# Performance work log

Measured on AMD Instinct MI355X. Metric: run time of the kernel, lower is better.

## Reference

```python
import jax, jax.numpy as jnp
import numpy as np

IN_FEATURES = 4096
OUT_FEATURES = 11008
GROUP_SIZE = 128
NUM_GROUPS = IN_FEATURES // GROUP_SIZE  # 32


def setup_inputs() -> dict:
    key = jax.random.key(0)
    k1, k2, k3, k4 = jax.random.split(key, 4)
    x = jax.random.normal(k1, (8192, IN_FEATURES), dtype=jnp.float32)
    # packed 4-bit weights: one uint8 byte holds two 4-bit values
    qweight = jax.random.randint(k2, (IN_FEATURES * OUT_FEATURES // 2,), 0, 256, dtype=jnp.int32)
    qzeros = jax.random.randint(k3, (OUT_FEATURES, NUM_GROUPS), 0, 16, dtype=jnp.int32)
    scales = jax.random.uniform(k4, (OUT_FEATURES, NUM_GROUPS), dtype=jnp.float32) * 0.01
    return {"x": x, "qweight": qweight, "qzeros": qzeros, "scales": scales}


def _dequantize(qweight, qzeros, scales):
    # unpack: low nibble first, then high nibble (matches stack([low, high], dim=1).view(-1))
    b = qweight.astype(jnp.int32)
    low = b & 15
    high = (b >> 4) & 15
    w = jnp.stack([low, high], axis=1).reshape(-1)  # [in*out]
    w = w[: OUT_FEATURES * IN_FEATURES].reshape(OUT_FEATURES, IN_FEATURES).astype(jnp.float32)
    # per-group dequant: (w - zero) * scale, groups along in_features
    w = w.reshape(OUT_FEATURES, NUM_GROUPS, GROUP_SIZE)
    w = (w - qzeros[:, :, None].astype(jnp.float32)) * scales[:, :, None]
    return w.reshape(OUT_FEATURES, IN_FEATURES)


def reference(x, qweight, qzeros, scales) -> jnp.ndarray:
    weight = _dequantize(qweight, qzeros, scales).astype(x.dtype)  # [out, in]
    # F.linear(x, W) = x @ W.T
    return jnp.einsum("bi,oi->bo", x, weight)
```

## Files before the change

### kernel.cpp

```cpp
#include <hip/hip_runtime.h>
#include <hip/hip_bf16.h>


#define IN_F   4096
#define OUT_F  11008
#define M_DIM  8192
#define NGROUP 32

typedef __bf16 bf16x8 __attribute__((ext_vector_type(8)));
typedef float  f32x4  __attribute__((ext_vector_type(4)));
typedef unsigned short u16;
typedef u16 u16x8v __attribute__((ext_vector_type(8)));

__device__ __forceinline__ u16 f2bf(float f) {
  union { float f; unsigned u; } v; v.f = f;
  unsigned u = v.u;
  return (u16)((u + 0x7fffu + ((u >> 16) & 1u)) >> 16);
}

__device__ __forceinline__ void gload_lds16(const void* gsrc, void* ldst) {
  __builtin_amdgcn_global_load_lds(
      (const __attribute__((address_space(1))) void*)gsrc,
      (__attribute__((address_space(3))) void*)ldst, 16, 0, 0);
}

__global__ __launch_bounds__(256) void dequant_w(const int* __restrict__ qw,
                                                 const int* __restrict__ qz,
                                                 const float* __restrict__ sc,
                                                 u16* __restrict__ W) {
  const int total = (IN_F / 2) * OUT_F / 4;
  int stride = gridDim.x * blockDim.x;
  for (int idx = blockIdx.x * blockDim.x + threadIdx.x; idx < total; idx += stride) {
    int j = idx << 2;
    int o = j >> 11;
    int g = (j >> 6) & 31;
    float z = (float)qz[(o << 5) + g];
    float s = sc[(o << 5) + g];
    int4 q = ((const int4*)qw)[idx];
    int qs0 = q.x, qs1 = q.y, qs2 = q.z, qs3 = q.w;
    u16x8v w;
    w[0] = f2bf(((float)(qs0 & 15) - z) * s);
    w[1] = f2bf(((float)((qs0 >> 4) & 15) - z) * s);
    w[2] = f2bf(((float)(qs1 & 15) - z) * s);
    w[3] = f2bf(((float)((qs1 >> 4) & 15) - z) * s);
    w[4] = f2bf(((float)(qs2 & 15) - z) * s);
    w[5] = f2bf(((float)((qs2 >> 4) & 15) - z) * s);
    w[6] = f2bf(((float)(qs3 & 15) - z) * s);
    w[7] = f2bf(((float)((qs3 >> 4) & 15) - z) * s);
    ((u16x8v*)W)[idx] = w;
  }
}

__global__ __launch_bounds__(256) void cvt_x(const float* __restrict__ x,
                                             u16* __restrict__ Xb) {
  const int total = M_DIM * IN_F / 8;
  int stride = gridDim.x * blockDim.x;
  for (int idx = blockIdx.x * blockDim.x + threadIdx.x; idx < total; idx += stride) {
    float4 a = ((const float4*)x)[idx * 2];
    float4 b = ((const float4*)x)[idx * 2 + 1];
    u16x8v v;
    v[0] = f2bf(a.x); v[1] = f2bf(a.y); v[2] = f2bf(a.z); v[3] = f2bf(a.w);
    v[4] = f2bf(b.x); v[5] = f2bf(b.y); v[6] = f2bf(b.z); v[7] = f2bf(b.w);
    ((u16x8v*)Xb)[idx] = v;
  }
}


#define BAR       __builtin_amdgcn_s_barrier()
#define LGKM0     asm volatile("s_waitcnt lgkmcnt(0)" ::: "memory")
#define VMCNT4    asm volatile("s_waitcnt vmcnt(4)" ::: "memory")
#define PRIO(p)   __builtin_amdgcn_s_setprio(p)

__global__ __launch_bounds__(512, 2) void gemm256(const u16* __restrict__ A,
                                                  const u16* __restrict__ B,
                                                  float* __restrict__ C) {
  constexpr int K = IN_F, N = OUT_F;
  constexpr int NT = K / 64;
  __shared__ __align__(16) u16 sA[2][256 * 64];
  __shared__ __align__(16) u16 sB[2][256 * 64];

  const int NTN = OUT_F / 256;
  const int NWG = (M_DIM / 256) * NTN;
  int bid = blockIdx.x;
  int wg  = (bid & 7) * (NWG / 8) + (bid >> 3);
  int tm = wg / NTN, tn = wg - tm * NTN;
  int m0 = tm * 256, n0 = tn * 256;

  int tid  = threadIdx.x;
  int lane = tid & 63;
  int wave = tid >> 6;
  int wr = wave >> 2, wc = wave & 3;

  int rstage = tid >> 3;
  int gslot  = ((tid & 7) ^ (rstage & 7)) << 3;
  int ldsoff = rstage * 64 + ((tid & 7) << 3);
  const u16* Ag = A + (size_t)(m0 + rstage) * K + gslot;
  const u16* Bg = B + (size_t)(n0 + rstage) * K + gslot;

#define STAGE_A(cb, h, kt) do {                                   \
    const u16* _g = Ag + (size_t)(h) * 128 * K + (kt) * 64;       \
    u16* _l = sA[cb] + (h) * 128 * 64 + ldsoff;                   \
    gload_lds16(_g, _l);                                          \
    gload_lds16(_g + (size_t)64 * K, _l + 64 * 64);               \
  } while (0)

#define STAGE_B(cb, h, kt) do {                                   \
    const u16* _g = Bg + (size_t)(h) * 128 * K + (kt) * 64;       \
    u16* _l = sB[cb] + (h) * 128 * 64 + ldsoff;                   \
    gload_lds16(_g, _l);                                          \
    gload_lds16(_g + (size_t)64 * K, _l + 64 * 64);               \
  } while (0)

  int q8  = lane >> 4;
  int sl0 = ((q8 ^ (lane & 7)) << 3);
  int sl1 = (((q8 | 4) ^ (lane & 7)) << 3);
  int abase = (wr * 128 + (lane & 15)) * 64;
  int bbase = (wc * 64 + (lane & 15)) * 64;

  bf16x8 a_[8], b0_[4], b1_[4];
  f32x4 acc[8][4] = {};

#define LDA(cb, mh) do {                                          \
    const u16* _p = sA[cb] + abase + (mh) * 4096;                 \
    a_[0] = *(const bf16x8*)(_p + sl0);                           \
    a_[1] = *(const bf16x8*)(_p + sl1);                           \
    a_[2] = *(const bf16x8*)(_p + 1024 + sl0);                    \
    a_[3] = *(const bf16x8*)(_p + 1024 + sl1);                    \
    a_[4] = *(const bf16x8*)(_p + 2048 + sl0);                    \
    a_[5] = *(const bf16x8*)(_p + 2048 + sl1);                    \
    a_[6] = *(const bf16x8*)(_p + 3072 + sl0);                    \
    a_[7] = *(const bf16x8*)(_p + 3072 + sl1);                    \
  } while (0)

#define LDB(cb, nh, dst) do {                                     \
    const u16* _p = sB[cb] + bbase + (nh) * 2048;                 \
    dst[0] = *(const bf16x8*)(_p + sl0);                          \
    dst[1] = *(const bf16x8*)(_p + sl1);                          \
    dst[2] = *(const bf16x8*)(_p + 1024 + sl0);                   \
    dst[3] = *(const bf16x8*)(_p + 1024 + sl1);                   \
  } while (0)

#define QUAD(mh, nh, bq) do {                                                  \
    _Pragma("unroll") for (int mf = 0; mf < 4; mf++)                           \
      _Pragma("unroll") for (int nf = 0; nf < 2; nf++) {                       \
        acc[(mh)*4+mf][(nh)*2+nf] = __builtin_amdgcn_mfma_f32_16x16x32_bf16(   \
            a_[mf*2+0], bq[nf*2+0], acc[(mh)*4+mf][(nh)*2+nf], 0, 0, 0);       \
        acc[(mh)*4+mf][(nh)*2+nf] = __builtin_amdgcn_mfma_f32_16x16x32_bf16(   \
            a_[mf*2+1], bq[nf*2+1], acc[(mh)*4+mf][(nh)*2+nf], 0, 0, 0);       \
      }                                                                        \
  } while (0)

#define TILE(c, u) do {                                           \
    int _ka = ((u) + 1) & (NT - 1), _kb = ((u) + 2) & (NT - 1);   \
                                                          \
    LDA(c, 0); LDB(c, 0, b0_); STAGE_A((c) ^ 1, 0, _ka);          \
    BAR; LGKM0; PRIO(1); QUAD(0, 0, b0_); PRIO(0); BAR;           \
                                                          \
    LDB(c, 1, b1_); STAGE_A((c) ^ 1, 1, _ka);                     \
    BAR; LGKM0; PRIO(1); QUAD(0, 1, b1_); PRIO(0); BAR;           \
                                                          \
    LDA(c, 1); STAGE_B(c, 0, _kb);                                \
    BAR; LGKM0; PRIO(1); QUAD(1, 1, b1_); PRIO(0); BAR;           \
                                                          \
    STAGE_B(c, 1, _kb);                                           \
    BAR; PRIO(1); QUAD(1, 0, b0_); PRIO(0); VMCNT4; BAR;          \
  } while (0)

  STAGE_A(0, 0, 0); STAGE_A(0, 1, 0);
  STAGE_B(0, 0, 0); STAGE_B(0, 1, 0);
  STAGE_B(1, 0, 1); STAGE_B(1, 1, 1);
  VMCNT4; BAR;

#pragma unroll 1
  for (int u = 0; u < NT; u += 2) {
    TILE(0, u);
    TILE(1, u + 1);
  }

  float* Cp = C + (size_t)(m0 + wr * 128 + ((lane >> 4) << 2)) * N + n0 + wc * 64 + (lane & 15);
#pragma unroll
  for (int m = 0; m < 8; m++)
#pragma unroll
    for (int n = 0; n < 4; n++)
#pragma unroll
      for (int j = 0; j < 4; j++)
        Cp[(size_t)(m * 16 + j) * N + n * 16] = acc[m][n][j];
}

__global__ __launch_bounds__(256) void naive_gemm(const float* __restrict__ x,
                                                  const int* __restrict__ qw,
                                                  const int* __restrict__ qz,
                                                  const float* __restrict__ sc,
                                                  float* __restrict__ out) {
  __shared__ float xs[IN_F];
  int m = blockIdx.y;
  int n = blockIdx.x * 256 + threadIdx.x;
  for (int i = threadIdx.x; i < IN_F; i += 256) xs[i] = x[(size_t)m * IN_F + i];
  __syncthreads();
  float acc = 0.f;
  const int* qrow = qw + (size_t)n * (IN_F / 2);
  for (int g = 0; g < NGROUP; g++) {
    float z = (float)qz[n * NGROUP + g];
    float s = sc[n * NGROUP + g];
    for (int t = 0; t < 64; t++) {
      int q = qrow[g * 64 + t];
      acc += xs[g * 128 + 2 * t] * ((float)(q & 15) - z) * s;
      acc += xs[g * 128 + 2 * t + 1] * ((float)((q >> 4) & 15) - z) * s;
    }
  }
  out[(size_t)m * OUT_F + n] = acc;
}

extern "C" void kernel_launch(void* const* d_in, const int* in_sizes, int n_in,
                              void* d_out, int out_size, void* d_ws, size_t ws_size,
                              hipStream_t stream) {
  const float* x  = (const float*)d_in[0];
  const int*   qw = (const int*)d_in[1];
  const int*   qz = (const int*)d_in[2];
  const float* sc = (const float*)d_in[3];
  float* out = (float*)d_out;

  const size_t WBYTES = (size_t)OUT_F * IN_F * 2;
  const size_t XBYTES = (size_t)M_DIM * IN_F * 2;

  if (ws_size >= WBYTES + XBYTES) {
    u16* Wb = (u16*)d_ws;
    u16* Xb = (u16*)((char*)d_ws + WBYTES);
    dequant_w<<<2048, 256, 0, stream>>>(qw, qz, sc, Wb);
    cvt_x<<<2048, 256, 0, stream>>>(x, Xb);
    gemm256<<<(M_DIM / 256) * (OUT_F / 256), 512, 0, stream>>>(Xb, Wb, out);
  } else {
    naive_gemm<<<dim3(OUT_F / 256, M_DIM), 256, 0, stream>>>(x, qw, qz, sc, out);
  }
}
```

Baseline: 771.9 us.

## Interleave warp tile ownership across halves and reschedule A/B staging pipeline

Each wave's fragments now come from both 128-row halves of the A and B tiles instead of one contiguous quadrant, so each stage-half is shared by all waves. The TILE schedule is reordered: the next tile's A upper half is prefetched earlier, the lower half is staged into the current buffer two tiles ahead, and waits move to lgkmcnt(8) and vmcnt(6). The aim is to overlap global-to-LDS traffic better with the MFMA quadrants. In exchange it adds buffer-reuse hazards: overwriting the current buffer's A half while other waves may still read it depends on exact barrier placement.

```diff
diff --git a/kernel.cpp b/kernel.cpp
--- a/kernel.cpp
+++ b/kernel.cpp
@@ -68,7 +68,8 @@
 
 #define BAR       __builtin_amdgcn_s_barrier()
 #define LGKM0     asm volatile("s_waitcnt lgkmcnt(0)" ::: "memory")
-#define VMCNT4    asm volatile("s_waitcnt vmcnt(4)" ::: "memory")
+#define LGKM8     asm volatile("s_waitcnt lgkmcnt(8)" ::: "memory")
+#define VMCNT6    asm volatile("s_waitcnt vmcnt(6)" ::: "memory")
 #define PRIO(p)   __builtin_amdgcn_s_setprio(p)
 
 __global__ __launch_bounds__(512, 2) void gemm256(const u16* __restrict__ A,
@@ -114,14 +115,14 @@
   int q8  = lane >> 4;
   int sl0 = ((q8 ^ (lane & 7)) << 3);
   int sl1 = (((q8 | 4) ^ (lane & 7)) << 3);
-  int abase = (wr * 128 + (lane & 15)) * 64;
-  int bbase = (wc * 64 + (lane & 15)) * 64;
+  int abase = (wr * 64 + (lane & 15)) * 64;
+  int bbase = (wc * 32 + (lane & 15)) * 64;
 
   bf16x8 a_[8], b0_[4], b1_[4];
   f32x4 acc[8][4] = {};
 
 #define LDA(cb, mh) do {                                          \
-    const u16* _p = sA[cb] + abase + (mh) * 4096;                 \
+    const u16* _p = sA[cb] + abase + (mh) * 8192;                 \
     a_[0] = *(const bf16x8*)(_p + sl0);                           \
     a_[1] = *(const bf16x8*)(_p + sl1);                           \
     a_[2] = *(const bf16x8*)(_p + 1024 + sl0);                    \
@@ -133,7 +134,7 @@
   } while (0)
 
 #define LDB(cb, nh, dst) do {                                     \
-    const u16* _p = sB[cb] + bbase + (nh) * 2048;                 \
+    const u16* _p = sB[cb] + bbase + (nh) * 8192;                 \
     dst[0] = *(const bf16x8*)(_p + sl0);                          \
     dst[1] = *(const bf16x8*)(_p + sl1);                          \
     dst[2] = *(const bf16x8*)(_p + 1024 + sl0);                   \
@@ -151,25 +152,25 @@
   } while (0)
 
 #define TILE(c, u) do {                                           \
-    int _ka = ((u) + 1) & (NT - 1), _kb = ((u) + 2) & (NT - 1);   \
-                                                          \
-    LDA(c, 0); LDB(c, 0, b0_); STAGE_A((c) ^ 1, 0, _ka);          \
-    BAR; LGKM0; PRIO(1); QUAD(0, 0, b0_); PRIO(0); BAR;           \
-                                                          \
-    LDB(c, 1, b1_); STAGE_A((c) ^ 1, 1, _ka);                     \
+    int _k1 = ((u) + 1) & (NT - 1), _k2 = ((u) + 2) & (NT - 1);   \
+                         \
+    LDA(c, 0); LDB(c, 0, b0_); STAGE_A((c) ^ 1, 1, _k1);          \
+    LGKM8; BAR; LGKM0; PRIO(1); QUAD(0, 0, b0_); PRIO(0); BAR;    \
+                           \
+    LDB(c, 1, b1_); STAGE_A(c, 0, _k2);                           \
     BAR; LGKM0; PRIO(1); QUAD(0, 1, b1_); PRIO(0); BAR;           \
-                                                          \
-    LDA(c, 1); STAGE_B(c, 0, _kb);                                \
+                           \
+    LDA(c, 1); STAGE_B(c, 0, _k2);                                \
     BAR; LGKM0; PRIO(1); QUAD(1, 1, b1_); PRIO(0); BAR;           \
-                                                          \
-    STAGE_B(c, 1, _kb);                                           \
-    BAR; PRIO(1); QUAD(1, 0, b0_); PRIO(0); VMCNT4; BAR;          \
+      \
+    STAGE_B(c, 1, _k2);                                           \
+    BAR; PRIO(1); QUAD(1, 0, b0_); PRIO(0); VMCNT6; BAR;          \
   } while (0)
 
   STAGE_A(0, 0, 0); STAGE_A(0, 1, 0);
   STAGE_B(0, 0, 0); STAGE_B(0, 1, 0);
-  STAGE_B(1, 0, 1); STAGE_B(1, 1, 1);
-  VMCNT4; BAR;
+  STAGE_A(1, 0, 1); STAGE_B(1, 0, 1); STAGE_B(1, 1, 1);
+  VMCNT6; BAR;
 
 #pragma unroll 1
   for (int u = 0; u < NT; u += 2) {
@@ -177,14 +178,19 @@
     TILE(1, u + 1);
   }
 
-  float* Cp = C + (size_t)(m0 + wr * 128 + ((lane >> 4) << 2)) * N + n0 + wc * 64 + (lane & 15);
+  float* Cp = C + (size_t)(m0 + wr * 64 + ((lane >> 4) << 2)) * N
+                + n0 + wc * 32 + (lane & 15);
 #pragma unroll
-  for (int m = 0; m < 8; m++)
+  for (int m = 0; m < 8; m++) {
+    int roff = (m >> 2) * 128 + (m & 3) * 16;
 #pragma unroll
-    for (int n = 0; n < 4; n++)
+    for (int n = 0; n < 4; n++) {
+      int coff = (n >> 1) * 128 + (n & 1) * 16;
 #pragma unroll
       for (int j = 0; j < 4; j++)
-        Cp[(size_t)(m * 16 + j) * N + n * 16] = acc[m][n][j];
+        Cp[(size_t)(roff + j) * N + coff] = acc[m][n][j];
+    }
+  }
 }
 
 __global__ __launch_bounds__(256) void naive_gemm(const float* __restrict__ x,
```

Measured after the change: 788.6 us. +2.2%, slower.

## Restructure GEMM main loop with double A fragment registers and reordered staging

Applied to the files above, without the earlier changes.

The bf16 MFMA GEMM main loop is reorganized: both halves of the A fragments are kept in registers (a0_/a1_), so each quadrant's MFMAs reuse loaded fragments in a snake order. The global-to-LDS staging schedule is also changed so that half-tiles of the next and next-next K step are interleaved differently, with adjusted prologue and waitcnt. Launch bounds drop from 2 to 1 workgroups per CU to allow more registers. The aim is fewer LDS reads and better overlap, at the risk of lower occupancy and possible staging hazards on buffers still being read.

```diff
diff --git a/kernel.cpp b/kernel.cpp
--- a/kernel.cpp
+++ b/kernel.cpp
@@ -67,11 +67,14 @@
 
 
 #define BAR       __builtin_amdgcn_s_barrier()
+#define SCHED0    __builtin_amdgcn_sched_barrier(0)
 #define LGKM0     asm volatile("s_waitcnt lgkmcnt(0)" ::: "memory")
+#define LGKM8     asm volatile("s_waitcnt lgkmcnt(8)" ::: "memory")
+#define VMCNT0    asm volatile("s_waitcnt vmcnt(0)" ::: "memory")
 #define VMCNT4    asm volatile("s_waitcnt vmcnt(4)" ::: "memory")
 #define PRIO(p)   __builtin_amdgcn_s_setprio(p)
 
-__global__ __launch_bounds__(512, 2) void gemm256(const u16* __restrict__ A,
+__global__ __launch_bounds__(512, 1) void gemm256(const u16* __restrict__ A,
                                                   const u16* __restrict__ B,
                                                   float* __restrict__ C) {
   constexpr int K = IN_F, N = OUT_F;
@@ -117,74 +120,82 @@
   int abase = (wr * 128 + (lane & 15)) * 64;
   int bbase = (wc * 64 + (lane & 15)) * 64;
 
-  bf16x8 a_[8], b0_[4], b1_[4];
+  bf16x8 a0_[8], a1_[8], b0_[4], b1_[4];
   f32x4 acc[8][4] = {};
 
-#define LDA(cb, mh) do {                                          \
+#define LDA_H(cb, mh, dst) do {                                   \
     const u16* _p = sA[cb] + abase + (mh) * 4096;                 \
-    a_[0] = *(const bf16x8*)(_p + sl0);                           \
-    a_[1] = *(const bf16x8*)(_p + sl1);                           \
-    a_[2] = *(const bf16x8*)(_p + 1024 + sl0);                    \
-    a_[3] = *(const bf16x8*)(_p + 1024 + sl1);                    \
-    a_[4] = *(const bf16x8*)(_p + 2048 + sl0);                    \
-    a_[5] = *(const bf16x8*)(_p + 2048 + sl1);                    \
-    a_[6] = *(const bf16x8*)(_p + 3072 + sl0);                    \
-    a_[7] = *(const bf16x8*)(_p + 3072 + sl1);                    \
-  } while (0)
-
-#define LDB(cb, nh, dst) do {                                     \
+    _Pragma("unroll") for (int mf = 0; mf < 4; mf++) {            \
+      dst[mf*2+0] = *(const bf16x8*)(_p + mf * 1024 + sl0);       \
+      dst[mf*2+1] = *(const bf16x8*)(_p + mf * 1024 + sl1);       \
+    }                                                             \
+  } while (0)
+
+#define LDB_H(cb, nh, dst) do {                                   \
     const u16* _p = sB[cb] + bbase + (nh) * 2048;                 \
-    dst[0] = *(const bf16x8*)(_p + sl0);                          \
-    dst[1] = *(const bf16x8*)(_p + sl1);                          \
-    dst[2] = *(const bf16x8*)(_p + 1024 + sl0);                   \
-    dst[3] = *(const bf16x8*)(_p + 1024 + sl1);                   \
-  } while (0)
-
-#define QUAD(mh, nh, bq) do {                                                  \
+    _Pragma("unroll") for (int nf = 0; nf < 2; nf++) {            \
+      dst[nf*2+0] = *(const bf16x8*)(_p + nf * 1024 + sl0);       \
+      dst[nf*2+1] = *(const bf16x8*)(_p + nf * 1024 + sl1);       \
+    }                                                             \
+  } while (0)
+
+#define QUAD16(aq, bq, mh, nh) do {                                            \
     _Pragma("unroll") for (int mf = 0; mf < 4; mf++)                           \
-      _Pragma("unroll") for (int nf = 0; nf < 2; nf++) {                       \
+      _Pragma("unroll") for (int nf = 0; nf < 2; nf++)                         \
         acc[(mh)*4+mf][(nh)*2+nf] = __builtin_amdgcn_mfma_f32_16x16x32_bf16(   \
-            a_[mf*2+0], bq[nf*2+0], acc[(mh)*4+mf][(nh)*2+nf], 0, 0, 0);       \
+            aq[mf*2+0], bq[nf*2+0], acc[(mh)*4+mf][(nh)*2+nf], 0, 0, 0);       \
+    _Pragma("unroll") for (int mf = 0; mf < 4; mf++)                           \
+      _Pragma("unroll") for (int nf = 0; nf < 2; nf++)                         \
         acc[(mh)*4+mf][(nh)*2+nf] = __builtin_amdgcn_mfma_f32_16x16x32_bf16(   \
-            a_[mf*2+1], bq[nf*2+1], acc[(mh)*4+mf][(nh)*2+nf], 0, 0, 0);       \
-      }                                                                        \
-  } while (0)
-
-#define TILE(c, u) do {                                           \
-    int _ka = ((u) + 1) & (NT - 1), _kb = ((u) + 2) & (NT - 1);   \
-                                                          \
-    LDA(c, 0); LDB(c, 0, b0_); STAGE_A((c) ^ 1, 0, _ka);          \
-    BAR; LGKM0; PRIO(1); QUAD(0, 0, b0_); PRIO(0); BAR;           \
-                                                          \
-    LDB(c, 1, b1_); STAGE_A((c) ^ 1, 1, _ka);                     \
-    BAR; LGKM0; PRIO(1); QUAD(0, 1, b1_); PRIO(0); BAR;           \
-                                                          \
-    LDA(c, 1); STAGE_B(c, 0, _kb);                                \
-    BAR; LGKM0; PRIO(1); QUAD(1, 1, b1_); PRIO(0); BAR;           \
-                                                          \
-    STAGE_B(c, 1, _kb);                                           \
-    BAR; PRIO(1); QUAD(1, 0, b0_); PRIO(0); VMCNT4; BAR;          \
+            aq[mf*2+1], bq[nf*2+1], acc[(mh)*4+mf][(nh)*2+nf], 0, 0, 0);       \
+  } while (0)
+
+#define TILE4(c, t) do {                                          \
+    int _k1 = ((t) + 1) & (NT - 1), _k2 = ((t) + 2) & (NT - 1);   \
+     \
+    LDA_H(c, 0, a0_); LDB_H(c, 0, b0_);                           \
+    STAGE_A((c) ^ 1, 1, _k1);                                     \
+    LGKM8; BAR; LGKM0;                                            \
+    PRIO(1); QUAD16(a0_, b0_, 0, 0); PRIO(0); BAR;                \
+               \
+    LDA_H(c, 1, a1_);                                             \
+    STAGE_B((c) ^ 1, 1, _k1);                                     \
+    BAR; LGKM0;                                                   \
+    PRIO(1); QUAD16(a1_, b0_, 1, 0); PRIO(0); BAR;                \
+        \
+    LDB_H(c, 1, b1_);                                             \
+    STAGE_A(c, 0, _k2);                                           \
+    BAR; LGKM0;                                                   \
+    PRIO(1); QUAD16(a1_, b1_, 1, 1); PRIO(0); BAR;                \
+       \
+    STAGE_B(c, 0, _k2);                                           \
+    BAR;                                                          \
+    PRIO(1); QUAD16(a0_, b1_, 0, 1); PRIO(0);                     \
+    VMCNT4; BAR;                                                  \
   } while (0)
 
   STAGE_A(0, 0, 0); STAGE_A(0, 1, 0);
   STAGE_B(0, 0, 0); STAGE_B(0, 1, 0);
-  STAGE_B(1, 0, 1); STAGE_B(1, 1, 1);
+  STAGE_A(1, 0, 1); STAGE_B(1, 0, 1);
   VMCNT4; BAR;
+  SCHED0;
+  asm volatile("" ::: "memory");
 
 #pragma unroll 1
-  for (int u = 0; u < NT; u += 2) {
-    TILE(0, u);
-    TILE(1, u + 1);
-  }
-
-  float* Cp = C + (size_t)(m0 + wr * 128 + ((lane >> 4) << 2)) * N + n0 + wc * 64 + (lane & 15);
+  for (int t = 0; t < NT; t += 2) {
+    TILE4(0, t);
+    TILE4(1, t + 1);
+  }
+
+  float* Cp = C + (size_t)(m0 + wr * 128 + ((lane >> 4) << 2)) * N
+                + n0 + wc * 64 + (lane & 15);
 #pragma unroll
-  for (int m = 0; m < 8; m++)
+  for (int mf = 0; mf < 8; mf++)
 #pragma unroll
-    for (int n = 0; n < 4; n++)
+    for (int nf = 0; nf < 4; nf++)
 #pragma unroll
       for (int j = 0; j < 4; j++)
-        Cp[(size_t)(m * 16 + j) * N + n * 16] = acc[m][n][j];
+        Cp[(size_t)(mf * 16 + j) * N + nf * 16] = acc[mf][nf][j];
 }
 
 __global__ __launch_bounds__(256) void naive_gemm(const float* __restrict__ x,
```

Measured after the change: 774.5 us. Within noise of the previous version (+0.3%).
